# Kernel tuning notes

Hardware: AMD Instinct MI355X
Metric: run time of the kernel (lower is better)

The kernel has to match this reference:

```python
import jax, jax.numpy as jnp
import numpy as np

N_NODES = 20000
N_EDGES = 160000
N_GRAPHS = 100
IN_CH = 64
EDGE_DIM = 8
NEG_SLOPE = 0.2


def _gatv2(x, edge_index, edge_attr, Wl, Wr, We, att, b, heads, ch, n_nodes):
    # GATv2Conv: e_ij = att . leaky_relu(Wl x_j + Wr x_i [+ We e_ij]), softmax over dst i,
    # out_i = sum_j alpha_ij * (Wl x_j), concat heads, + bias.
    src, dst = edge_index[0], edge_index[1]
    xl = (x @ Wl).reshape(-1, heads, ch)  # [N,H,C] source-side transform
    xr = (x @ Wr).reshape(-1, heads, ch)  # [N,H,C] target-side transform
    m = xl[src] + xr[dst]                 # [E,H,C]
    if edge_attr is not None:
        m = m + (edge_attr @ We).reshape(-1, heads, ch)
    m = jax.nn.leaky_relu(m, NEG_SLOPE)
    logit = jnp.einsum('ehc,hc->eh', m, att)                     # [E,H]
    mx = jax.ops.segment_max(logit, dst, num_segments=n_nodes)   # [N,H]
    ex = jnp.exp(logit - mx[dst])
    den = jax.ops.segment_sum(ex, dst, num_segments=n_nodes)     # [N,H]
    alpha = ex / (den[dst] + 1e-16)                              # [E,H]
    out = jax.ops.segment_sum(alpha[:, :, None] * xl[src], dst, num_segments=n_nodes)
    return out.reshape(-1, heads * ch) + b


def setup_inputs() -> dict:
    key = jax.random.key(0)
    ks = jax.random.split(key, 24)
    def rn(k, shape, fan_in):
        return jax.random.normal(k, shape, dtype=jnp.float32) / np.sqrt(fan_in)
    inp = {}
    inp['x'] = jax.random.normal(ks[0], (N_NODES, IN_CH), dtype=jnp.float32)
    inp['edge_attr'] = jax.random.uniform(ks[1], (N_EDGES, EDGE_DIM), dtype=jnp.float32)
    inp['Wl1'] = rn(ks[2], (IN_CH, 1024), IN_CH)
    inp['Wr1'] = rn(ks[3], (IN_CH, 1024), IN_CH)
    inp['We1'] = rn(ks[4], (EDGE_DIM, 1024), EDGE_DIM)
    inp['att1'] = rn(ks[5], (4, 256), 256)
    inp['b1'] = jnp.zeros((1024,), jnp.float32)
    inp['Wl2'] = rn(ks[6], (1024, 256), 1024)
    inp['Wr2'] = rn(ks[7], (1024, 256), 1024)
    inp['We2'] = rn(ks[8], (EDGE_DIM, 256), EDGE_DIM)
    inp['att2'] = rn(ks[9], (4, 64), 64)
    inp['b2'] = jnp.zeros((256,), jnp.float32)
    inp['Wlp'] = rn(ks[10], (256, 384), 256)
    inp['Wrp'] = rn(ks[11], (256, 384), 256)
    inp['attp'] = rn(ks[12], (6, 64), 64)
    inp['bp'] = jnp.zeros((384,), jnp.float32)
    inp['Wfc1'] = rn(ks[13], (384, 64), 384)
    inp['bfc1'] = jnp.zeros((64,), jnp.float32)
    inp['Wfc2'] = rn(ks[14], (64, 1), 64)
    inp['bfc2'] = jnp.zeros((1,), jnp.float32)
    inp['edge_index'] = jax.random.randint(ks[15], (2, N_EDGES), 0, N_NODES, dtype=jnp.int32)
    inp['edge_index_master'] = jax.random.randint(ks[16], (2, N_EDGES), 0, N_NODES, dtype=jnp.int32)
    inp['n_nodes'] = jnp.full((N_GRAPHS,), N_NODES // N_GRAPHS, dtype=jnp.int32)
    return inp


def reference(x, edge_attr, Wl1, Wr1, We1, att1, b1, Wl2, Wr2, We2, att2, b2,
              Wlp, Wrp, attp, bp, Wfc1, bfc1, Wfc2, bfc2,
              edge_index, edge_index_master, n_nodes):
    h = _gatv2(x, edge_index, edge_attr, Wl1, Wr1, We1, att1, b1, 4, 256, N_NODES)
    h = jax.nn.relu(h)
    h = _gatv2(h, edge_index, edge_attr, Wl2, Wr2, We2, att2, b2, 4, 64, N_NODES)
    h = jax.nn.relu(h)
    h = _gatv2(h, edge_index_master, None, Wlp, Wrp, None, attp, bp, 6, 64, N_NODES)
    last_idx = jnp.cumsum(n_nodes) - 1          # master node = last node of each graph
    master = h[last_idx]                        # [G,384] (dropout p=0 -> identity)
    z = jax.nn.relu(master @ Wfc1 + bfc1)
    return z @ Wfc2 + bfc2                      # [G,1]
```

## Files before the change

### kernel.cpp

```cpp
#include <hip/hip_runtime.h>
#include <hip/hip_bf16.h>

#define DIV_UP(a,b) (((a)+(b)-1)/(b))

typedef __attribute__((ext_vector_type(8))) short short8;
typedef __attribute__((ext_vector_type(4))) float floatx4;

static __device__ __forceinline__ unsigned short f2bf(float v) {
    unsigned u = __builtin_bit_cast(unsigned, v);
    u += 0x7fffu + ((u >> 16) & 1u);
    return (unsigned short)(u >> 16);
}
static __device__ __forceinline__ float bflo(unsigned v) {
    return __builtin_bit_cast(float, v << 16);
}
static __device__ __forceinline__ float bfhi(unsigned v) {
    return __builtin_bit_cast(float, v & 0xffff0000u);
}

template <int CPL>
static __device__ __forceinline__ void load_bf16v(const unsigned short* p, float* d) {
    if constexpr (CPL == 8) {
        uint4 v = *(const uint4*)p;
        d[0] = bflo(v.x); d[1] = bfhi(v.x);
        d[2] = bflo(v.y); d[3] = bfhi(v.y);
        d[4] = bflo(v.z); d[5] = bfhi(v.z);
        d[6] = bflo(v.w); d[7] = bfhi(v.w);
    } else if constexpr (CPL == 4) {
        uint2 v = *(const uint2*)p;
        d[0] = bflo(v.x); d[1] = bfhi(v.x);
        d[2] = bflo(v.y); d[3] = bfhi(v.y);
    } else if constexpr (CPL == 2) {
        unsigned v = *(const unsigned*)p;
        d[0] = bflo(v); d[1] = bfhi(v);
    } else {
        d[0] = bflo(*p);
    }
}

template <int CPL>
static __device__ __forceinline__ void store_bf16v(unsigned short* p, const float* s) {
    unsigned short tmp[CPL];
#pragma unroll
    for (int c = 0; c < CPL; ++c) tmp[c] = f2bf(s[c]);
    if constexpr (CPL == 8) *(uint4*)p = *(uint4*)tmp;
    else if constexpr (CPL == 4) *(ushort4*)p = *(ushort4*)tmp;
    else if constexpr (CPL == 2) *(ushort2*)p = *(ushort2*)tmp;
    else p[0] = tmp[0];
}

template <int CTRL>
static __device__ __forceinline__ float dpp_mv(float x) {
    int r = __builtin_amdgcn_update_dpp(0, __builtin_bit_cast(int, x), CTRL, 0xF, 0xF, false);
    return __builtin_bit_cast(float, r);
}
template <int G>
static __device__ __forceinline__ float group_reduce(float x) {
    x += dpp_mv<0xB1>(x);
    x += dpp_mv<0x4E>(x);
    x += dpp_mv<0x124>(x);
    x += dpp_mv<0x128>(x);
    if constexpr (G >= 32) x += __shfl_xor(x, 16, 64);
    if constexpr (G >= 64) x += __shfl_xor(x, 32, 64);
    return x;
}

static __device__ __forceinline__ void tr_pair(const float* Wa, const float* Wb, int K, int Nn,
                                               unsigned short* Wt, int i) {
    int tot = K * Nn;
    const float* W = (i < tot) ? Wa : Wb;
    unsigned short* dst = Wt + ((i < tot) ? 0 : (size_t)Nn * K);
    int ii = (i < tot) ? i : i - tot;
    int k = ii % K, n = ii / K;
    dst[(size_t)n * K + k] = f2bf(W[(size_t)k * Nn + n]);
}

__global__ void prep_all(const float* __restrict__ x,
                         const float* __restrict__ Wl1, const float* __restrict__ Wr1,
                         const float* __restrict__ Wl2, const float* __restrict__ Wr2,
                         const float* __restrict__ Wlp, const float* __restrict__ Wrp,
                         unsigned short* __restrict__ xbf,
                         unsigned short* __restrict__ wt1, unsigned short* __restrict__ wt2,
                         unsigned short* __restrict__ wt3, int N) {
    const int S1 = 2 * 64 * 1024, S2 = 2 * 1024 * 256, S3 = 2 * 256 * 384;
    int id = blockIdx.x * blockDim.x + threadIdx.x;
    if (id < S1) tr_pair(Wl1, Wr1, 64, 1024, wt1, id);
    else if (id < S1 + S2) tr_pair(Wl2, Wr2, 1024, 256, wt2, id - S1);
    else if (id < S1 + S2 + S3) tr_pair(Wlp, Wrp, 256, 384, wt3, id - S1 - S2);
    else {
        int i = id - S1 - S2 - S3;
        if (i < N * 64) xbf[i] = f2bf(x[i]);
    }
}

__global__ __launch_bounds__(256) void gemm_mfma(
    const unsigned short* __restrict__ A, const unsigned short* __restrict__ Bt,
    unsigned short* __restrict__ C, int M, int Ntot, int K) {
    constexpr int LDA = 40;
    __shared__ unsigned short As[128 * LDA];
    __shared__ unsigned short Bs[128 * LDA];
    const int tid = threadIdx.x;
    const int m0 = blockIdx.y * 128, n0 = blockIdx.x * 128;
    const int wave = tid >> 6, lane = tid & 63;
    const int wm = (wave >> 1) * 64, wn = (wave & 1) * 64;
    const int r15 = lane & 15, quad = lane >> 4;
    const int sr = tid >> 1, skc = tid & 1;
    floatx4 acc[4][4];
#pragma unroll
    for (int i = 0; i < 4; ++i)
#pragma unroll
        for (int j = 0; j < 4; ++j) acc[i][j] = (floatx4)0.f;

    for (int k0 = 0; k0 < K; k0 += 32) {
        uint4 a0 = make_uint4(0, 0, 0, 0), a1 = make_uint4(0, 0, 0, 0);
        int am = m0 + sr;
        if (am < M) {
            const unsigned short* ap = A + (size_t)am * K + k0 + skc * 16;
            a0 = *(const uint4*)ap;
            a1 = *(const uint4*)(ap + 8);
        }
        const unsigned short* bp = Bt + (size_t)(n0 + sr) * K + k0 + skc * 16;
        uint4 b0 = *(const uint4*)bp;
        uint4 b1 = *(const uint4*)(bp + 8);
        *(uint4*)(&As[sr * LDA + skc * 16]) = a0;
        *(uint4*)(&As[sr * LDA + skc * 16 + 8]) = a1;
        *(uint4*)(&Bs[sr * LDA + skc * 16]) = b0;
        *(uint4*)(&Bs[sr * LDA + skc * 16 + 8]) = b1;
        __syncthreads();
        short8 af[4], bfr[4];
#pragma unroll
        for (int i = 0; i < 4; ++i)
            af[i] = *(const short8*)(&As[(wm + i * 16 + r15) * LDA + quad * 8]);
#pragma unroll
        for (int j = 0; j < 4; ++j)
            bfr[j] = *(const short8*)(&Bs[(wn + j * 16 + r15) * LDA + quad * 8]);
#pragma unroll
        for (int i = 0; i < 4; ++i)
#pragma unroll
            for (int j = 0; j < 4; ++j)
                acc[i][j] = __builtin_amdgcn_mfma_f32_16x16x32_bf16(af[i], bfr[j], acc[i][j], 0, 0, 0);
        __syncthreads();
    }
#pragma unroll
    for (int i = 0; i < 4; ++i)
#pragma unroll
        for (int j = 0; j < 4; ++j)
#pragma unroll
            for (int r = 0; r < 4; ++r) {
                int m = m0 + wm + i * 16 + quad * 4 + r;
                int n = n0 + wn + j * 16 + r15;
                if (m < M) C[(size_t)m * Ntot + n] = f2bf(acc[i][j][r]);
            }
}

__global__ void count2_kernel(const int* __restrict__ dst0, const int* __restrict__ dst1,
                              int E, int N, int* __restrict__ cnt) {
    int e = blockIdx.x * blockDim.x + threadIdx.x;
    if (e < E) atomicAdd(&cnt[dst0[e]], 1);
    else if (e < 2 * E) atomicAdd(&cnt[N + dst1[e - E]], 1);
}

__global__ __launch_bounds__(1024) void scan_kernel(const int* __restrict__ cnt_all, int N,
                                                    int* __restrict__ off_all, int* __restrict__ cur_all) {
    const int* cnt = cnt_all + blockIdx.x * N;
    int* off = off_all + blockIdx.x * (N + 1);
    int* cur = cur_all + blockIdx.x * N;
    __shared__ int part[1024];
    int t = threadIdx.x;
    int per = (N + 1023) >> 10;
    int base = t * per;
    int s = 0;
    for (int i = 0; i < per; ++i) { int idx = base + i; if (idx < N) s += cnt[idx]; }
    part[t] = s;
    __syncthreads();
    for (int d2 = 1; d2 < 1024; d2 <<= 1) {
        int v = (t >= d2) ? part[t - d2] : 0;
        __syncthreads();
        part[t] += v;
        __syncthreads();
    }
    int pre = (t == 0) ? 0 : part[t - 1];
    for (int i = 0; i < per; ++i) {
        int idx = base + i;
        if (idx < N) { off[idx] = pre; cur[idx] = pre; pre += cnt[idx]; }
    }
    if (t == 1023) off[N] = part[1023];
}

__global__ void fill2_kernel(const int* __restrict__ src0, const int* __restrict__ dst0,
                             const int* __restrict__ src1, const int* __restrict__ dst1,
                             int E, int N, int* __restrict__ cur, int2* __restrict__ edges) {
    int e = blockIdx.x * blockDim.x + threadIdx.x;
    if (e < E) {
        int p = atomicAdd(&cur[dst0[e]], 1);
        edges[p] = make_int2(src0[e], e);
    } else if (e < 2 * E) {
        int i = e - E;
        int p = atomicAdd(&cur[N + dst1[i]], 1);
        edges[E + p] = make_int2(src1[i], i);
    }
}

template <int D, int CPL, int QP, int G, int NE>
static __device__ __forceinline__ void hase_group(
    const unsigned short* __restrict__ xlr, const float* __restrict__ ea,
    const float* wb, const float (&att_r)[CPL], const float (&xr_r)[CPL],
    const int2* ep , int c0,
    float& m, float& l, float (&acc)[CPL]) {
    int2 e[NE];
#pragma unroll
    for (int n = 0; n < NE; ++n) e[n] = ep[n];
    float ev[NE][8];
#pragma unroll
    for (int n = 0; n < NE; ++n) {
        float4 a = ((const float4*)(ea + (size_t)e[n].y * 8))[0];
        float4 b = ((const float4*)(ea + (size_t)e[n].y * 8))[1];
        ev[n][0] = a.x; ev[n][1] = a.y; ev[n][2] = a.z; ev[n][3] = a.w;
        ev[n][4] = b.x; ev[n][5] = b.y; ev[n][6] = b.z; ev[n][7] = b.w;
    }
    float xv[NE][CPL], z[NE][CPL];
#pragma unroll
    for (int n = 0; n < NE; ++n) {
        load_bf16v<CPL>(xlr + (size_t)e[n].x * (2 * D) + c0, xv[n]);
#pragma unroll
        for (int c = 0; c < CPL; ++c) z[n][c] = xv[n][c] + xr_r[c];
    }
#pragma unroll
    for (int k = 0; k < 8; ++k) {
#pragma unroll
        for (int q = 0; q < CPL / 4; ++q) {
            float4 w4 = *(const float4*)(wb + k * D + q * QP);
#pragma unroll
            for (int n = 0; n < NE; ++n) {
                z[n][q * 4 + 0] = fmaf(ev[n][k], w4.x, z[n][q * 4 + 0]);
                z[n][q * 4 + 1] = fmaf(ev[n][k], w4.y, z[n][q * 4 + 1]);
                z[n][q * 4 + 2] = fmaf(ev[n][k], w4.z, z[n][q * 4 + 2]);
                z[n][q * 4 + 3] = fmaf(ev[n][k], w4.w, z[n][q * 4 + 3]);
            }
        }
    }
    float lg[NE];
#pragma unroll
    for (int n = 0; n < NE; ++n) {
        lg[n] = 0.f;
#pragma unroll
        for (int c = 0; c < CPL; ++c) {
            float a = z[n][c] > 0.f ? z[n][c] : 0.2f * z[n][c];
            lg[n] = fmaf(att_r[c], a, lg[n]);
        }
        lg[n] = group_reduce<G>(lg[n]);
    }
    float mn = m;
#pragma unroll
    for (int n = 0; n < NE; ++n) mn = fmaxf(mn, lg[n]);
    float sc = __expf(m - mn);
    float p[NE], ps = 0.f;
#pragma unroll
    for (int n = 0; n < NE; ++n) { p[n] = __expf(lg[n] - mn); ps += p[n]; }
    m = mn;
    l = fmaf(l, sc, ps);
#pragma unroll
    for (int c = 0; c < CPL; ++c) {
        float t = p[0] * xv[0][c];
#pragma unroll
        for (int n = 1; n < NE; ++n) t = fmaf(p[n], xv[n][c], t);
        acc[c] = fmaf(acc[c], sc, t);
    }
}

template <int D, int C, int CB, int WPN, bool RELU>
__global__ __launch_bounds__(256) void attn_hase(
    const unsigned short* __restrict__ xlr, const float* __restrict__ ea,
    const float* __restrict__ We, const float* __restrict__ att,
    const int2* __restrict__ edges, const int* __restrict__ off,
    const float* __restrict__ bias, unsigned short* __restrict__ outp, int N) {
    constexpr int CPL = CB / 64;
    constexpr int HW = CB / C;
    constexpr int G = 64 / HW;
    constexpr int NPB = 4 / WPN;
    constexpr int QP = CB * 4 / CPL;
    __shared__ float wsh[8 * D];
    for (int f4 = threadIdx.x; f4 < 2 * D; f4 += 256) {
        int k = f4 / (D / 4);
        int c = (f4 - k * (D / 4)) * 4;
        int b = c / CB, cc = c - b * CB;
        int ln = cc / CPL, q = (cc % CPL) / 4;
        int dst = k * (D / 4) + (b * CB + q * QP + ln * 4) / 4;
        ((float4*)wsh)[dst] = ((const float4*)We)[f4];
    }
    __syncthreads();

    const int wid = threadIdx.x >> 6, lane = threadIdx.x & 63;
    const int wv = wid % WPN, wn = wid / WPN;
    const int c0 = wv * CB + lane * CPL;
    const float* wb = wsh + wv * CB + lane * 4;

    float att_r[CPL];
#pragma unroll
    for (int c = 0; c < CPL; ++c) att_r[c] = att[c0 + c];

    for (int node = blockIdx.x * NPB + wn; node < N; node += gridDim.x * NPB) {
        float xr_r[CPL];
        load_bf16v<CPL>(xlr + (size_t)node * (2 * D) + D + c0, xr_r);
        float m = -1e30f, l = 0.f, acc[CPL];
#pragma unroll
        for (int c = 0; c < CPL; ++c) acc[c] = 0.f;

        const int jb = __builtin_amdgcn_readfirstlane(off[node]);
        const int je = __builtin_amdgcn_readfirstlane(off[node + 1]);
        int j = jb;
        for (; j + 4 <= je; j += 4)
            hase_group<D, CPL, QP, G, 4>(xlr, ea, wb, att_r, xr_r, edges + j, c0, m, l, acc);
        for (; j < je; ++j)
            hase_group<D, CPL, QP, G, 1>(xlr, ea, wb, att_r, xr_r, edges + j, c0, m, l, acc);

        float inv = 1.f / (l + 1e-16f);
        float r[CPL];
#pragma unroll
        for (int c = 0; c < CPL; ++c) {
            r[c] = fmaf(acc[c], inv, bias[c0 + c]);
            if constexpr (RELU) r[c] = fmaxf(r[c], 0.f);
        }
        store_bf16v<CPL>(outp + (size_t)node * D + c0, r);
    }
}

template <int D, int CPL, int G, int NE>
static __device__ __forceinline__ void noe_group(
    const unsigned short* __restrict__ xlr,
    const float (&att_r)[CPL], const float (&xr_r)[CPL],
    const int2* ep , int c0,
    float& m, float& l, float (&acc)[CPL]) {
    int2 e[NE];
#pragma unroll
    for (int n = 0; n < NE; ++n) e[n] = ep[n];
    float xv[NE][CPL], lg[NE];
#pragma unroll
    for (int n = 0; n < NE; ++n)
        load_bf16v<CPL>(xlr + (size_t)e[n].x * (2 * D) + c0, xv[n]);
#pragma unroll
    for (int n = 0; n < NE; ++n) {
        lg[n] = 0.f;
#pragma unroll
        for (int c = 0; c < CPL; ++c) {
            float z = xv[n][c] + xr_r[c];
            z = z > 0.f ? z : 0.2f * z;
            lg[n] = fmaf(att_r[c], z, lg[n]);
        }
        lg[n] = group_reduce<G>(lg[n]);
    }
    float mn = m;
#pragma unroll
    for (int n = 0; n < NE; ++n) mn = fmaxf(mn, lg[n]);
    float sc = __expf(m - mn);
    float p[NE], ps = 0.f;
#pragma unroll
    for (int n = 0; n < NE; ++n) { p[n] = __expf(lg[n] - mn); ps += p[n]; }
    m = mn;
    l = fmaf(l, sc, ps);
#pragma unroll
    for (int c = 0; c < CPL; ++c) {
        float t = p[0] * xv[0][c];
#pragma unroll
        for (int n = 1; n < NE; ++n) t = fmaf(p[n], xv[n][c], t);
        acc[c] = fmaf(acc[c], sc, t);
    }
}

template <int D, int C, int CB, bool RELU>
static __device__ __forceinline__ void attn_wave3(
    const unsigned short* __restrict__ xlr, const float* __restrict__ att,
    const int2* __restrict__ edges, int jb, int je,
    const float* __restrict__ bias, float* __restrict__ outp,
    int node, int cb, int lane) {
    constexpr int CPL = CB / 64;
    constexpr int HW = CB / C;
    constexpr int G = 64 / HW;
    const int c0 = cb + lane * CPL;

    float xr_r[CPL], att_r[CPL];
    load_bf16v<CPL>(xlr + (size_t)node * (2 * D) + D + c0, xr_r);
#pragma unroll
    for (int c = 0; c < CPL; ++c) att_r[c] = att[c0 + c];

    float m = -1e30f, l = 0.f, acc[CPL];
#pragma unroll
    for (int c = 0; c < CPL; ++c) acc[c] = 0.f;

    int j = jb;
    for (; j + 4 <= je; j += 4)
        noe_group<D, CPL, G, 4>(xlr, att_r, xr_r, edges + j, c0, m, l, acc);
    for (; j < je; ++j)
        noe_group<D, CPL, G, 1>(xlr, att_r, xr_r, edges + j, c0, m, l, acc);

    float inv = 1.f / (l + 1e-16f);
    float* out = outp + (size_t)node * D + c0;
    float tmp[CPL];
#pragma unroll
    for (int c = 0; c < CPL; ++c) {
        float r = fmaf(acc[c], inv, bias[c0 + c]);
        if constexpr (RELU) r = fmaxf(r, 0.f);
        tmp[c] = r;
    }
    if constexpr (CPL == 4) *(float4*)out = *(float4*)tmp;
    else if constexpr (CPL == 2) *(float2*)out = *(float2*)tmp;
    else out[0] = tmp[0];
}

template <int D, int C, int CB0, int CB1, bool RELU>
__global__ __launch_bounds__(256) void attn_noe(
    const unsigned short* __restrict__ xlr, const float* __restrict__ att,
    const int2* __restrict__ edges, const int* __restrict__ off,
    const float* __restrict__ bias, float* __restrict__ outp, int N) {
    const int wid = threadIdx.x >> 6, lane = threadIdx.x & 63;
    const int gw = blockIdx.x * 4 + wid;
    const int node = gw >> 1, wv = gw & 1;
    if (node >= N) return;
    const int jb = __builtin_amdgcn_readfirstlane(off[node]);
    const int je = __builtin_amdgcn_readfirstlane(off[node + 1]);
    if (wv == 0)
        attn_wave3<D, C, CB0, RELU>(xlr, att, edges, jb, je, bias, outp, node, 0, lane);
    else
        attn_wave3<D, C, CB1, RELU>(xlr, att, edges, jb, je, bias, outp, node, CB0, lane);
}

__global__ void mlp_kernel(const float* __restrict__ h3, const int* __restrict__ nn,
                           const float* __restrict__ Wfc1, const float* __restrict__ bfc1,
                           const float* __restrict__ Wfc2, const float* __restrict__ bfc2,
                           float* __restrict__ out, int G) {
    int g = blockIdx.x, t = threadIdx.x;
    int s = 0;
    for (int k = 0; k <= g; ++k) s += nn[k];
    const float* row = h3 + (size_t)(s - 1) * 384;
    float z = bfc1[t];
    for (int k = 0; k < 384; ++k) z = fmaf(row[k], Wfc1[k * 64 + t], z);
    z = fmaxf(z, 0.f);
    float v = z * Wfc2[t];
#pragma unroll
    for (int o = 32; o; o >>= 1) v += __shfl_xor(v, o, 64);
    if (t == 0) out[g] = v + bfc2[0];
}

extern "C" void kernel_launch(void* const* d_in, const int* in_sizes, int n_in,
                              void* d_out, int out_size, void* d_ws, size_t ws_size,
                              hipStream_t stream) {
    const float* x    = (const float*)d_in[0];
    const float* ea   = (const float*)d_in[1];
    const float* Wl1  = (const float*)d_in[2];
    const float* Wr1  = (const float*)d_in[3];
    const float* We1  = (const float*)d_in[4];
    const float* att1 = (const float*)d_in[5];
    const float* b1   = (const float*)d_in[6];
    const float* Wl2  = (const float*)d_in[7];
    const float* Wr2  = (const float*)d_in[8];
    const float* We2  = (const float*)d_in[9];
    const float* att2 = (const float*)d_in[10];
    const float* b2   = (const float*)d_in[11];
    const float* Wlp  = (const float*)d_in[12];
    const float* Wrp  = (const float*)d_in[13];
    const float* attp = (const float*)d_in[14];
    const float* bp   = (const float*)d_in[15];
    const float* Wfc1 = (const float*)d_in[16];
    const float* bfc1 = (const float*)d_in[17];
    const float* Wfc2 = (const float*)d_in[18];
    const float* bfc2 = (const float*)d_in[19];
    const int* ei     = (const int*)d_in[20];
    const int* eim    = (const int*)d_in[21];
    const int* nn     = (const int*)d_in[22];

    const int N = in_sizes[0] / 64;
    const int E = in_sizes[20] / 2;
    const int G = in_sizes[22];
    const int* src1 = ei,  *dst1 = ei + E;
    const int* srcm = eim, *dstm = eim + E;

    char* w = (char*)d_ws;
    size_t o = 0;
    auto alloc = [&](size_t b) { size_t r = o; o += (b + 255) & ~(size_t)255; return r; };
    char* R1 = w + alloc((size_t)N * 2048 * 2);
    unsigned short* xlr1 = (unsigned short*)R1;
    unsigned short* xlr3 = (unsigned short*)R1;
    float* h3 = (float*)(R1 + (size_t)N * 768 * 2 + 256);
    unsigned short* h1   = (unsigned short*)(w + alloc((size_t)N * 1024 * 2));
    unsigned short* xlr2 = (unsigned short*)(w + alloc((size_t)N * 512 * 2));
    unsigned short* h2   = (unsigned short*)(w + alloc((size_t)N * 256 * 2));
    unsigned short* xbf  = (unsigned short*)(w + alloc((size_t)N * 64 * 2));
    unsigned short* wt1  = (unsigned short*)(w + alloc((size_t)2048 * 64 * 2));
    unsigned short* wt2  = (unsigned short*)(w + alloc((size_t)512 * 1024 * 2));
    unsigned short* wt3  = (unsigned short*)(w + alloc((size_t)768 * 256 * 2));
    int*  cnt   = (int*)(w + alloc((size_t)2 * N * 4));
    int*  off   = (int*)(w + alloc((size_t)2 * (N + 1) * 4));
    int*  cur   = (int*)(w + alloc((size_t)2 * N * 4));
    int2* edges = (int2*)(w + alloc((size_t)2 * E * 8 + 4096));
    (void)ws_size; (void)n_in; (void)out_size;

    dim3 blk(256);

    {
        int tot = 2 * 64 * 1024 + 2 * 1024 * 256 + 2 * 256 * 384 + N * 64;
        prep_all<<<DIV_UP(tot, 256), blk, 0, stream>>>(x, Wl1, Wr1, Wl2, Wr2, Wlp, Wrp,
                                                       xbf, wt1, wt2, wt3, N);
    }

    hipMemsetAsync(cnt, 0, (size_t)2 * N * 4, stream);
    count2_kernel<<<DIV_UP(2 * E, 256), blk, 0, stream>>>(dst1, dstm, E, N, cnt);
    scan_kernel<<<2, 1024, 0, stream>>>(cnt, N, off, cur);
    fill2_kernel<<<DIV_UP(2 * E, 256), blk, 0, stream>>>(src1, dst1, srcm, dstm, E, N, cur, edges);
    const int* off3 = off + (N + 1);
    int2* edges3 = edges + E;

    gemm_mfma<<<dim3(2048 / 128, DIV_UP(N, 128)), blk, 0, stream>>>(xbf, wt1, xlr1, N, 2048, 64);
    attn_hase<1024, 256, 512, 2, true><<<2560, blk, 0, stream>>>(
        xlr1, ea, We1, att1, edges, off, b1, h1, N);

    gemm_mfma<<<dim3(512 / 128, DIV_UP(N, 128)), blk, 0, stream>>>(h1, wt2, xlr2, N, 512, 1024);
    attn_hase<256, 64, 256, 1, true><<<1280, blk, 0, stream>>>(
        xlr2, ea, We2, att2, edges, off, b2, h2, N);

    gemm_mfma<<<dim3(768 / 128, DIV_UP(N, 128)), blk, 0, stream>>>(h2, wt3, xlr3, N, 768, 256);
    attn_noe<384, 64, 256, 128, false><<<DIV_UP(N, 2), blk, 0, stream>>>(
        xlr3, attp, edges3, off3, bp, h3, N);

    mlp_kernel<<<G, 64, 0, stream>>>(h3, nn, Wfc1, bfc1, Wfc2, bfc2, (float*)d_out, G);
}
```

Before: 423.5 us.

## Use packed f32x2 math in attention kernels and one-wave-per-node third layer

Rewrites the per-edge attention math in the GATv2 aggregation kernels to use two-wide float vectors, so the compiler can emit packed FMA/max instructions on MI355X. The third-layer kernel changes from two waves per node (256+128 channels) to a single wave per node, with 48 active lanes each handling 8 channels. A group reduction over 8 lanes is added for that case. This halves wave count and edge-index/offset traffic for layer 3, but leaves 16 lanes idle and doubles per-lane register and load width.

```diff
diff --git a/kernel.cpp b/kernel.cpp
--- a/kernel.cpp
+++ b/kernel.cpp
@@ -5,6 +5,7 @@
 
 typedef __attribute__((ext_vector_type(8))) short short8;
 typedef __attribute__((ext_vector_type(4))) float floatx4;
+typedef __attribute__((ext_vector_type(2))) float f32x2;
 
 static __device__ __forceinline__ unsigned short f2bf(float v) {
     unsigned u = __builtin_bit_cast(unsigned, v);
@@ -17,36 +18,42 @@
 static __device__ __forceinline__ float bfhi(unsigned v) {
     return __builtin_bit_cast(float, v & 0xffff0000u);
 }
+static __device__ __forceinline__ f32x2 mk2(float a, float b) {
+    f32x2 r; r.x = a; r.y = b; return r;
+}
+static __device__ __forceinline__ f32x2 splat2(float a) {
+    f32x2 r; r.x = a; r.y = a; return r;
+}
 
 template <int CPL>
-static __device__ __forceinline__ void load_bf16v(const unsigned short* p, float* d) {
+static __device__ __forceinline__ void load_bf16p(const unsigned short* p, f32x2* d) {
     if constexpr (CPL == 8) {
         uint4 v = *(const uint4*)p;
-        d[0] = bflo(v.x); d[1] = bfhi(v.x);
-        d[2] = bflo(v.y); d[3] = bfhi(v.y);
-        d[4] = bflo(v.z); d[5] = bfhi(v.z);
-        d[6] = bflo(v.w); d[7] = bfhi(v.w);
+        d[0] = mk2(bflo(v.x), bfhi(v.x));
+        d[1] = mk2(bflo(v.y), bfhi(v.y));
+        d[2] = mk2(bflo(v.z), bfhi(v.z));
+        d[3] = mk2(bflo(v.w), bfhi(v.w));
     } else if constexpr (CPL == 4) {
         uint2 v = *(const uint2*)p;
-        d[0] = bflo(v.x); d[1] = bfhi(v.x);
-        d[2] = bflo(v.y); d[3] = bfhi(v.y);
-    } else if constexpr (CPL == 2) {
+        d[0] = mk2(bflo(v.x), bfhi(v.x));
+        d[1] = mk2(bflo(v.y), bfhi(v.y));
+    } else {
         unsigned v = *(const unsigned*)p;
-        d[0] = bflo(v); d[1] = bfhi(v);
-    } else {
-        d[0] = bflo(*p);
+        d[0] = mk2(bflo(v), bfhi(v));
     }
 }
 
 template <int CPL>
-static __device__ __forceinline__ void store_bf16v(unsigned short* p, const float* s) {
+static __device__ __forceinline__ void store_bf16p(unsigned short* p, const f32x2* s) {
     unsigned short tmp[CPL];
 #pragma unroll
-    for (int c = 0; c < CPL; ++c) tmp[c] = f2bf(s[c]);
+    for (int c = 0; c < CPL / 2; ++c) {
+        tmp[2 * c] = f2bf(s[c].x);
+        tmp[2 * c + 1] = f2bf(s[c].y);
+    }
     if constexpr (CPL == 8) *(uint4*)p = *(uint4*)tmp;
     else if constexpr (CPL == 4) *(ushort4*)p = *(ushort4*)tmp;
-    else if constexpr (CPL == 2) *(ushort2*)p = *(ushort2*)tmp;
-    else p[0] = tmp[0];
+    else *(ushort2*)p = *(ushort2*)tmp;
 }
 
 template <int CTRL>
@@ -58,10 +65,14 @@
 static __device__ __forceinline__ float group_reduce(float x) {
     x += dpp_mv<0xB1>(x);
     x += dpp_mv<0x4E>(x);
-    x += dpp_mv<0x124>(x);
-    x += dpp_mv<0x128>(x);
-    if constexpr (G >= 32) x += __shfl_xor(x, 16, 64);
-    if constexpr (G >= 64) x += __shfl_xor(x, 32, 64);
+    if constexpr (G == 8) {
+        x += __shfl_xor(x, 4, 64);
+    } else if constexpr (G >= 16) {
+        x += dpp_mv<0x124>(x);
+        x += dpp_mv<0x128>(x);
+        if constexpr (G >= 32) x += __shfl_xor(x, 16, 64);
+        if constexpr (G >= 64) x += __shfl_xor(x, 32, 64);
+    }
     return x;
 }
 
@@ -204,9 +215,10 @@
 template <int D, int CPL, int QP, int G, int NE>
 static __device__ __forceinline__ void hase_group(
     const unsigned short* __restrict__ xlr, const float* __restrict__ ea,
-    const float* wb, const float (&att_r)[CPL], const float (&xr_r)[CPL],
+    const float* wb, const f32x2 (&att2)[CPL / 2], const f32x2 (&xr2)[CPL / 2],
     const int2* ep , int c0,
-    float& m, float& l, float (&acc)[CPL]) {
+    float& m, float& l, f32x2 (&acc2)[CPL / 2]) {
+    constexpr int C2 = CPL / 2;
     int2 e[NE];
 #pragma unroll
     for (int n = 0; n < NE; ++n) e[n] = ep[n];
@@ -218,37 +230,37 @@
         ev[n][0] = a.x; ev[n][1] = a.y; ev[n][2] = a.z; ev[n][3] = a.w;
         ev[n][4] = b.x; ev[n][5] = b.y; ev[n][6] = b.z; ev[n][7] = b.w;
     }
-    float xv[NE][CPL], z[NE][CPL];
+    f32x2 xv2[NE][C2], z2[NE][C2];
 #pragma unroll
     for (int n = 0; n < NE; ++n) {
-        load_bf16v<CPL>(xlr + (size_t)e[n].x * (2 * D) + c0, xv[n]);
-#pragma unroll
-        for (int c = 0; c < CPL; ++c) z[n][c] = xv[n][c] + xr_r[c];
+        load_bf16p<CPL>(xlr + (size_t)e[n].x * (2 * D) + c0, xv2[n]);
+#pragma unroll
+        for (int c = 0; c < C2; ++c) z2[n][c] = xv2[n][c] + xr2[c];
     }
 #pragma unroll
     for (int k = 0; k < 8; ++k) {
 #pragma unroll
         for (int q = 0; q < CPL / 4; ++q) {
             float4 w4 = *(const float4*)(wb + k * D + q * QP);
+            f32x2 wa = mk2(w4.x, w4.y), wc = mk2(w4.z, w4.w);
 #pragma unroll
             for (int n = 0; n < NE; ++n) {
-                z[n][q * 4 + 0] = fmaf(ev[n][k], w4.x, z[n][q * 4 + 0]);
-                z[n][q * 4 + 1] = fmaf(ev[n][k], w4.y, z[n][q * 4 + 1]);
-                z[n][q * 4 + 2] = fmaf(ev[n][k], w4.z, z[n][q * 4 + 2]);
-                z[n][q * 4 + 3] = fmaf(ev[n][k], w4.w, z[n][q * 4 + 3]);
+                f32x2 es = splat2(ev[n][k]);
+                z2[n][2 * q] = __builtin_elementwise_fma(es, wa, z2[n][2 * q]);
+                z2[n][2 * q + 1] = __builtin_elementwise_fma(es, wc, z2[n][2 * q + 1]);
             }
         }
     }
     float lg[NE];
 #pragma unroll
     for (int n = 0; n < NE; ++n) {
-        lg[n] = 0.f;
-#pragma unroll
-        for (int c = 0; c < CPL; ++c) {
-            float a = z[n][c] > 0.f ? z[n][c] : 0.2f * z[n][c];
-            lg[n] = fmaf(att_r[c], a, lg[n]);
+        f32x2 lg2 = splat2(0.f);
+#pragma unroll
+        for (int c = 0; c < C2; ++c) {
+            f32x2 a2 = __builtin_elementwise_max(z2[n][c], z2[n][c] * 0.2f);
+            lg2 = __builtin_elementwise_fma(att2[c], a2, lg2);
         }
-        lg[n] = group_reduce<G>(lg[n]);
+        lg[n] = group_reduce<G>(lg2.x + lg2.y);
     }
     float mn = m;
 #pragma unroll
@@ -259,12 +271,13 @@
     for (int n = 0; n < NE; ++n) { p[n] = __expf(lg[n] - mn); ps += p[n]; }
     m = mn;
     l = fmaf(l, sc, ps);
-#pragma unroll
-    for (int c = 0; c < CPL; ++c) {
-        float t = p[0] * xv[0][c];
-#pragma unroll
-        for (int n = 1; n < NE; ++n) t = fmaf(p[n], xv[n][c], t);
-        acc[c] = fmaf(acc[c], sc, t);
+    f32x2 scs = splat2(sc);
+#pragma unroll
+    for (int c = 0; c < C2; ++c) {
+        f32x2 t = xv2[0][c] * p[0];
+#pragma unroll
+        for (int n = 1; n < NE; ++n) t = __builtin_elementwise_fma(splat2(p[n]), xv2[n][c], t);
+        acc2[c] = __builtin_elementwise_fma(acc2[c], scs, t);
     }
 }
 
@@ -295,59 +308,63 @@
     const int c0 = wv * CB + lane * CPL;
     const float* wb = wsh + wv * CB + lane * 4;
 
-    float att_r[CPL];
-#pragma unroll
-    for (int c = 0; c < CPL; ++c) att_r[c] = att[c0 + c];
+    f32x2 att2[CPL / 2];
+#pragma unroll
+    for (int c = 0; c < CPL / 2; ++c) att2[c] = mk2(att[c0 + 2 * c], att[c0 + 2 * c + 1]);
 
     for (int node = blockIdx.x * NPB + wn; node < N; node += gridDim.x * NPB) {
-        float xr_r[CPL];
-        load_bf16v<CPL>(xlr + (size_t)node * (2 * D) + D + c0, xr_r);
-        float m = -1e30f, l = 0.f, acc[CPL];
-#pragma unroll
-        for (int c = 0; c < CPL; ++c) acc[c] = 0.f;
+        f32x2 xr2[CPL / 2];
+        load_bf16p<CPL>(xlr + (size_t)node * (2 * D) + D + c0, xr2);
+        float m = -1e30f, l = 0.f;
+        f32x2 acc2[CPL / 2];
+#pragma unroll
+        for (int c = 0; c < CPL / 2; ++c) acc2[c] = splat2(0.f);
 
         const int jb = __builtin_amdgcn_readfirstlane(off[node]);
         const int je = __builtin_amdgcn_readfirstlane(off[node + 1]);
         int j = jb;
         for (; j + 4 <= je; j += 4)
-            hase_group<D, CPL, QP, G, 4>(xlr, ea, wb, att_r, xr_r, edges + j, c0, m, l, acc);
+            hase_group<D, CPL, QP, G, 4>(xlr, ea, wb, att2, xr2, edges + j, c0, m, l, acc2);
         for (; j < je; ++j)
-            hase_group<D, CPL, QP, G, 1>(xlr, ea, wb, att_r, xr_r, edges + j, c0, m, l, acc);
-
-        float inv = 1.f / (l + 1e-16f);
-        float r[CPL];
-#pragma unroll
-        for (int c = 0; c < CPL; ++c) {
-            r[c] = fmaf(acc[c], inv, bias[c0 + c]);
-            if constexpr (RELU) r[c] = fmaxf(r[c], 0.f);
+            hase_group<D, CPL, QP, G, 1>(xlr, ea, wb, att2, xr2, edges + j, c0, m, l, acc2);
+
+        f32x2 invs = splat2(1.f / (l + 1e-16f));
+        f32x2 r2[CPL / 2];
+#pragma unroll
+        for (int c = 0; c < CPL / 2; ++c) {
+            f32x2 b2 = mk2(bias[c0 + 2 * c], bias[c0 + 2 * c + 1]);
+            r2[c] = __builtin_elementwise_fma(acc2[c], invs, b2);
+            if constexpr (RELU) r2[c] = __builtin_elementwise_max(r2[c], splat2(0.f));
         }
-        store_bf16v<CPL>(outp + (size_t)node * D + c0, r);
+        store_bf16p<CPL>(outp + (size_t)node * D + c0, r2);
     }
 }
 
 template <int D, int CPL, int G, int NE>
 static __device__ __forceinline__ void noe_group(
     const unsigned short* __restrict__ xlr,
-    const float (&att_r)[CPL], const float (&xr_r)[CPL],
+    const f32x2 (&att2)[CPL / 2], const f32x2 (&xr2)[CPL / 2],
     const int2* ep , int c0,
-    float& m, float& l, float (&acc)[CPL]) {
+    float& m, float& l, f32x2 (&acc2)[CPL / 2]) {
+    constexpr int C2 = CPL / 2;
     int2 e[NE];
 #pragma unroll
     for (int n = 0; n < NE; ++n) e[n] = ep[n];
-    float xv[NE][CPL], lg[NE];
+    f32x2 xv2[NE][C2];
+    float lg[NE];
 #pragma unroll
     for (int n = 0; n < NE; ++n)
-        load_bf16v<CPL>(xlr + (size_t)e[n].x * (2 * D) + c0, xv[n]);
+        load_bf16p<CPL>(xlr + (size_t)e[n].x * (2 * D) + c0, xv2[n]);
 #pragma unroll
     for (int n = 0; n < NE; ++n) {
-        lg[n] = 0.f;
-#pragma unroll
-        for (int c = 0; c < CPL; ++c) {
-            float z = xv[n][c] + xr_r[c];
-            z = z > 0.f ? z : 0.2f * z;
-            lg[n] = fmaf(att_r[c], z, lg[n]);
+        f32x2 lg2 = splat2(0.f);
+#pragma unroll
+        for (int c = 0; c < C2; ++c) {
+            f32x2 z = xv2[n][c] + xr2[c];
+            f32x2 a2 = __builtin_elementwise_max(z, z * 0.2f);
+            lg2 = __builtin_elementwise_fma(att2[c], a2, lg2);
         }
-        lg[n] = group_reduce<G>(lg[n]);
+        lg[n] = group_reduce<G>(lg2.x + lg2.y);
     }
     float mn = m;
 #pragma unroll
@@ -358,70 +375,69 @@
     for (int n = 0; n < NE; ++n) { p[n] = __expf(lg[n] - mn); ps += p[n]; }
     m = mn;
     l = fmaf(l, sc, ps);
-#pragma unroll
-    for (int c = 0; c < CPL; ++c) {
-        float t = p[0] * xv[0][c];
-#pragma unroll
-        for (int n = 1; n < NE; ++n) t = fmaf(p[n], xv[n][c], t);
-        acc[c] = fmaf(acc[c], sc, t);
-    }
-}
-
-template <int D, int C, int CB, bool RELU>
-static __device__ __forceinline__ void attn_wave3(
-    const unsigned short* __restrict__ xlr, const float* __restrict__ att,
-    const int2* __restrict__ edges, int jb, int je,
-    const float* __restrict__ bias, float* __restrict__ outp,
-    int node, int cb, int lane) {
-    constexpr int CPL = CB / 64;
-    constexpr int HW = CB / C;
-    constexpr int G = 64 / HW;
-    const int c0 = cb + lane * CPL;
-
-    float xr_r[CPL], att_r[CPL];
-    load_bf16v<CPL>(xlr + (size_t)node * (2 * D) + D + c0, xr_r);
-#pragma unroll
-    for (int c = 0; c < CPL; ++c) att_r[c] = att[c0 + c];
-
-    float m = -1e30f, l = 0.f, acc[CPL];
-#pragma unroll
-    for (int c = 0; c < CPL; ++c) acc[c] = 0.f;
-
-    int j = jb;
-    for (; j + 4 <= je; j += 4)
-        noe_group<D, CPL, G, 4>(xlr, att_r, xr_r, edges + j, c0, m, l, acc);
-    for (; j < je; ++j)
-        noe_group<D, CPL, G, 1>(xlr, att_r, xr_r, edges + j, c0, m, l, acc);
-
-    float inv = 1.f / (l + 1e-16f);
-    float* out = outp + (size_t)node * D + c0;
-    float tmp[CPL];
-#pragma unroll
-    for (int c = 0; c < CPL; ++c) {
-        float r = fmaf(acc[c], inv, bias[c0 + c]);
-        if constexpr (RELU) r = fmaxf(r, 0.f);
-        tmp[c] = r;
-    }
-    if constexpr (CPL == 4) *(float4*)out = *(float4*)tmp;
-    else if constexpr (CPL == 2) *(float2*)out = *(float2*)tmp;
-    else out[0] = tmp[0];
-}
-
-template <int D, int C, int CB0, int CB1, bool RELU>
-__global__ __launch_bounds__(256) void attn_noe(
+    f32x2 scs = splat2(sc);
+#pragma unroll
+    for (int c = 0; c < C2; ++c) {
+        f32x2 t = xv2[0][c] * p[0];
+#pragma unroll
+        for (int n = 1; n < NE; ++n) t = __builtin_elementwise_fma(splat2(p[n]), xv2[n][c], t);
+        acc2[c] = __builtin_elementwise_fma(acc2[c], scs, t);
+    }
+}
+
+template <int D, int C, int CPL, bool RELU>
+__global__ __launch_bounds__(256) void attn_noe1(
     const unsigned short* __restrict__ xlr, const float* __restrict__ att,
     const int2* __restrict__ edges, const int* __restrict__ off,
     const float* __restrict__ bias, float* __restrict__ outp, int N) {
+    constexpr int ACT = D / CPL;
+    constexpr int G = C / CPL;
     const int wid = threadIdx.x >> 6, lane = threadIdx.x & 63;
-    const int gw = blockIdx.x * 4 + wid;
-    const int node = gw >> 1, wv = gw & 1;
-    if (node >= N) return;
+    const int node = blockIdx.x * 4 + wid;
+    if (node >= N || lane >= ACT) return;
+    const int c0 = lane * CPL;
+
+    f32x2 att2[CPL / 2], xr2[CPL / 2];
+#pragma unroll
+    for (int c = 0; c < CPL / 2; ++c) att2[c] = mk2(att[c0 + 2 * c], att[c0 + 2 * c + 1]);
+    load_bf16p<CPL>(xlr + (size_t)node * (2 * D) + D + c0, xr2);
+
+    float m = -1e30f, l = 0.f;
+    f32x2 acc2[CPL / 2];
+#pragma unroll
+    for (int c = 0; c < CPL / 2; ++c) acc2[c] = splat2(0.f);
+
     const int jb = __builtin_amdgcn_readfirstlane(off[node]);
     const int je = __builtin_amdgcn_readfirstlane(off[node + 1]);
-    if (wv == 0)
-        attn_wave3<D, C, CB0, RELU>(xlr, att, edges, jb, je, bias, outp, node, 0, lane);
-    else
-        attn_wave3<D, C, CB1, RELU>(xlr, att, edges, jb, je, bias, outp, node, CB0, lane);
+    int j = jb;
+    for (; j + 4 <= je; j += 4)
+        noe_group<D, CPL, G, 4>(xlr, att2, xr2, edges + j, c0, m, l, acc2);
+    for (; j < je; ++j)
+        noe_group<D, CPL, G, 1>(xlr, att2, xr2, edges + j, c0, m, l, acc2);
+
+    f32x2 invs = splat2(1.f / (l + 1e-16f));
+    float* out = outp + (size_t)node * D + c0;
+    float4 o0, o1;
+    {
+        f32x2 b0 = mk2(bias[c0 + 0], bias[c0 + 1]);
+        f32x2 b1 = mk2(bias[c0 + 2], bias[c0 + 3]);
+        f32x2 b2 = mk2(bias[c0 + 4], bias[c0 + 5]);
+        f32x2 b3 = mk2(bias[c0 + 6], bias[c0 + 7]);
+        f32x2 r0 = __builtin_elementwise_fma(acc2[0], invs, b0);
+        f32x2 r1 = __builtin_elementwise_fma(acc2[1], invs, b1);
+        f32x2 r2 = __builtin_elementwise_fma(acc2[2], invs, b2);
+        f32x2 r3 = __builtin_elementwise_fma(acc2[3], invs, b3);
+        if constexpr (RELU) {
+            r0 = __builtin_elementwise_max(r0, splat2(0.f));
+            r1 = __builtin_elementwise_max(r1, splat2(0.f));
+            r2 = __builtin_elementwise_max(r2, splat2(0.f));
+            r3 = __builtin_elementwise_max(r3, splat2(0.f));
+        }
+        o0 = make_float4(r0.x, r0.y, r1.x, r1.y);
+        o1 = make_float4(r2.x, r2.y, r3.x, r3.y);
+    }
+    *(float4*)out = o0;
+    *(float4*)(out + 4) = o1;
 }
 
 __global__ void mlp_kernel(const float* __restrict__ h3, const int* __restrict__ nn,
@@ -518,7 +534,7 @@
         xlr2, ea, We2, att2, edges, off, b2, h2, N);
 
     gemm_mfma<<<dim3(768 / 128, DIV_UP(N, 128)), blk, 0, stream>>>(h2, wt3, xlr3, N, 768, 256);
-    attn_noe<384, 64, 256, 128, false><<<DIV_UP(N, 2), blk, 0, stream>>>(
+    attn_noe1<384, 64, 8, false><<<DIV_UP(N, 4), blk, 0, stream>>>(
         xlr3, attp, edges3, off3, bp, h3, N);
 
     mlp_kernel<<<G, 64, 0, stream>>>(h3, nn, Wfc1, bfc1, Wfc2, bfc2, (float*)d_out, G);
```

New measurement: 430.2 us. About the same (+1.6%).

## Process third-layer attention with one wave per node using eight channels per lane

Applied to the files above, without the earlier changes.

The no-edge-attr attention kernel for the pooling layer now assigns a whole node to a single wave. Each of 48 active lanes handles 8 channels, replacing the previous split across two waves with 4 and 2 channels per lane. This halves the number of waves and the duplicated edge-index and offset loads, and it loads wider 16-byte vectors. The head reduction for 8-lane groups now uses a shuffle with xor 4 instead of row-level DPP ops. In exchange, 16 lanes per wave sit idle and each lane holds more register state, which may lower latency hiding.

```diff
diff --git a/kernel.cpp b/kernel.cpp
--- a/kernel.cpp
+++ b/kernel.cpp
@@ -58,10 +58,14 @@
 static __device__ __forceinline__ float group_reduce(float x) {
     x += dpp_mv<0xB1>(x);
     x += dpp_mv<0x4E>(x);
-    x += dpp_mv<0x124>(x);
-    x += dpp_mv<0x128>(x);
-    if constexpr (G >= 32) x += __shfl_xor(x, 16, 64);
-    if constexpr (G >= 64) x += __shfl_xor(x, 32, 64);
+    if constexpr (G == 8) {
+        x += __shfl_xor(x, 4, 64);
+    } else if constexpr (G >= 16) {
+        x += dpp_mv<0x124>(x);
+        x += dpp_mv<0x128>(x);
+        if constexpr (G >= 32) x += __shfl_xor(x, 16, 64);
+        if constexpr (G >= 64) x += __shfl_xor(x, 32, 64);
+    }
     return x;
 }
 
@@ -367,26 +371,29 @@
     }
 }
 
-template <int D, int C, int CB, bool RELU>
-static __device__ __forceinline__ void attn_wave3(
+template <int D, int C, int CPL, bool RELU>
+__global__ __launch_bounds__(256) void attn_noe1(
     const unsigned short* __restrict__ xlr, const float* __restrict__ att,
-    const int2* __restrict__ edges, int jb, int je,
-    const float* __restrict__ bias, float* __restrict__ outp,
-    int node, int cb, int lane) {
-    constexpr int CPL = CB / 64;
-    constexpr int HW = CB / C;
-    constexpr int G = 64 / HW;
-    const int c0 = cb + lane * CPL;
-
-    float xr_r[CPL], att_r[CPL];
+    const int2* __restrict__ edges, const int* __restrict__ off,
+    const float* __restrict__ bias, float* __restrict__ outp, int N) {
+    constexpr int ACT = D / CPL;
+    constexpr int G = C / CPL;
+    const int wid = threadIdx.x >> 6, lane = threadIdx.x & 63;
+    const int node = blockIdx.x * 4 + wid;
+    if (node >= N || lane >= ACT) return;
+    const int c0 = lane * CPL;
+
+    float att_r[CPL], xr_r[CPL];
+#pragma unroll
+    for (int c = 0; c < CPL; ++c) att_r[c] = att[c0 + c];
     load_bf16v<CPL>(xlr + (size_t)node * (2 * D) + D + c0, xr_r);
-#pragma unroll
-    for (int c = 0; c < CPL; ++c) att_r[c] = att[c0 + c];
 
     float m = -1e30f, l = 0.f, acc[CPL];
 #pragma unroll
     for (int c = 0; c < CPL; ++c) acc[c] = 0.f;
 
+    const int jb = __builtin_amdgcn_readfirstlane(off[node]);
+    const int je = __builtin_amdgcn_readfirstlane(off[node + 1]);
     int j = jb;
     for (; j + 4 <= je; j += 4)
         noe_group<D, CPL, G, 4>(xlr, att_r, xr_r, edges + j, c0, m, l, acc);
@@ -398,30 +405,11 @@
     float tmp[CPL];
 #pragma unroll
     for (int c = 0; c < CPL; ++c) {
-        float r = fmaf(acc[c], inv, bias[c0 + c]);
-        if constexpr (RELU) r = fmaxf(r, 0.f);
-        tmp[c] = r;
-    }
-    if constexpr (CPL == 4) *(float4*)out = *(float4*)tmp;
-    else if constexpr (CPL == 2) *(float2*)out = *(float2*)tmp;
-    else out[0] = tmp[0];
-}
-
-template <int D, int C, int CB0, int CB1, bool RELU>
-__global__ __launch_bounds__(256) void attn_noe(
-    const unsigned short* __restrict__ xlr, const float* __restrict__ att,
-    const int2* __restrict__ edges, const int* __restrict__ off,
-    const float* __restrict__ bias, float* __restrict__ outp, int N) {
-    const int wid = threadIdx.x >> 6, lane = threadIdx.x & 63;
-    const int gw = blockIdx.x * 4 + wid;
-    const int node = gw >> 1, wv = gw & 1;
-    if (node >= N) return;
-    const int jb = __builtin_amdgcn_readfirstlane(off[node]);
-    const int je = __builtin_amdgcn_readfirstlane(off[node + 1]);
-    if (wv == 0)
-        attn_wave3<D, C, CB0, RELU>(xlr, att, edges, jb, je, bias, outp, node, 0, lane);
-    else
-        attn_wave3<D, C, CB1, RELU>(xlr, att, edges, jb, je, bias, outp, node, CB0, lane);
+        tmp[c] = fmaf(acc[c], inv, bias[c0 + c]);
+        if constexpr (RELU) tmp[c] = fmaxf(tmp[c], 0.f);
+    }
+    *(float4*)out = make_float4(tmp[0], tmp[1], tmp[2], tmp[3]);
+    *(float4*)(out + 4) = make_float4(tmp[4], tmp[5], tmp[6], tmp[7]);
 }
 
 __global__ void mlp_kernel(const float* __restrict__ h3, const int* __restrict__ nn,
@@ -518,7 +506,7 @@
         xlr2, ea, We2, att2, edges, off, b2, h2, N);
 
     gemm_mfma<<<dim3(768 / 128, DIV_UP(N, 128)), blk, 0, stream>>>(h2, wt3, xlr3, N, 768, 256);
-    attn_noe<384, 64, 256, 128, false><<<DIV_UP(N, 2), blk, 0, stream>>>(
+    attn_noe1<384, 64, 8, false><<<DIV_UP(N, 4), blk, 0, stream>>>(
         xlr3, attp, edges3, off3, bp, h3, N);
 
     mlp_kernel<<<G, 64, 0, stream>>>(h3, nn, Wfc1, bfc1, Wfc2, bfc2, (float*)d_out, G);
```

Result: no change. 424.7 us (median of 2 runs) (+0.3%).
